# Kernel optimization log

Measured on AMD Instinct MI355X. Metric: run time of the kernel, lower is better.

The kernel has to match this reference:

```python
import jax, jax.numpy as jnp
import numpy as np

B, S, D_MODEL, D_FF = 4, 2048, 1024, 4096


def setup_inputs() -> dict:
    key = jax.random.key(0)
    ks = jax.random.split(key, 8)
    return {
        "x": jax.random.normal(ks[0], (B, S, D_MODEL), dtype=jnp.float32),
        "W1": jax.random.normal(ks[1], (D_MODEL, D_FF), dtype=jnp.float32) * (1.0 / np.sqrt(D_MODEL)),
        "b1": jnp.zeros((D_FF,), dtype=jnp.float32),
        "quantum_phases": jax.random.normal(ks[2], (D_FF,), dtype=jnp.float32) * (2.0 * np.pi),
        "quantum_weights_real": jax.random.normal(ks[3], (D_FF,), dtype=jnp.float32) * 0.1,
        "quantum_weights_imag": jax.random.normal(ks[4], (D_FF,), dtype=jnp.float32) * 0.1,
        "W2": jax.random.normal(ks[5], (D_FF, D_MODEL), dtype=jnp.float32) * (1.0 / np.sqrt(D_FF)),
        "b2": jnp.zeros((D_MODEL,), dtype=jnp.float32),
    }


def _quantum_transform(hidden, theta, w_real, w_imag):
    # hidden: [B,S,d_ff]; theta/w_real/w_imag: [d_ff] broadcast over channels
    imag = w_imag * jnp.sin(theta + hidden * 0.1)
    quantum_phase = jnp.cos(theta) * w_real + jnp.sin(theta) * w_imag  # [d_ff]
    return hidden + quantum_phase * imag * 0.1


def reference(x, W1, b1, quantum_phases, quantum_weights_real, quantum_weights_imag, W2, b2):
    hidden = jnp.einsum("bsd,df->bsf", x, W1) + b1  # [B,S,d_ff]
    q = _quantum_transform(hidden, quantum_phases, quantum_weights_real, quantum_weights_imag)
    act = jax.nn.relu(q)  # dropout is identity in eval mode
    return jnp.einsum("bsf,fd->bsd", act, W2) + b2
```

## Files before the change

kernel.cpp:

```cpp
#include <hip/hip_runtime.h>

typedef __bf16 bf16x8 __attribute__((ext_vector_type(8)));
typedef short  s16x8  __attribute__((ext_vector_type(8)));
typedef float  f32x4  __attribute__((ext_vector_type(4)));

#define DEVINL __device__ __forceinline__

DEVINL unsigned short f2bf(float f) {
  unsigned int u = __builtin_bit_cast(unsigned int, f);
  u += 0x7fffu + ((u >> 16) & 1u);
  return (unsigned short)(u >> 16);
}

DEVINL void async16(const void* g, void* l) {
  __builtin_amdgcn_global_load_lds(
      (const __attribute__((address_space(1))) unsigned int*)g,
      (__attribute__((address_space(3))) unsigned int*)l, 16, 0, 0);
}


__global__ void cvt_f32_bf16(const float* __restrict__ in,
                             unsigned short* __restrict__ out, int n4) {
  int i = blockIdx.x * blockDim.x + threadIdx.x;
  int stride = gridDim.x * blockDim.x;
  for (; i < n4; i += stride) {
    float4 v = ((const float4*)in)[i];
    ushort4 o;
    o.x = f2bf(v.x); o.y = f2bf(v.y); o.z = f2bf(v.z); o.w = f2bf(v.w);
    ((ushort4*)out)[i] = o;
  }
}

__global__ void transpose_cvt(const float* __restrict__ in,
                              unsigned short* __restrict__ out, int R, int C) {
  __shared__ unsigned short tile[32][33];
  int bc = blockIdx.x * 32, br = blockIdx.y * 32;
  int tx = threadIdx.x & 31, ty = threadIdx.x >> 5;
#pragma unroll
  for (int i = 0; i < 32; i += 8)
    tile[ty + i][tx] = f2bf(in[(size_t)(br + ty + i) * C + (bc + tx)]);
  __syncthreads();
#pragma unroll
  for (int i = 0; i < 32; i += 8)
    out[(size_t)(bc + ty + i) * R + (br + tx)] = tile[tx][ty + i];
}

__global__ void qconst(const float* __restrict__ theta,
                       const float* __restrict__ wre,
                       const float* __restrict__ wim,
                       float* __restrict__ c1, int n) {
  int i = blockIdx.x * blockDim.x + threadIdx.x;
  if (i < n) {
    float t = theta[i];
    c1[i] = (cosf(t) * wre[i] + sinf(t) * wim[i]) * wim[i] * 0.1f;
  }
}


template <int BM, int NT, int REPS, bool FUSED>
__global__ __launch_bounds__(512, 2) void gemm8(
    const unsigned short* __restrict__ A,
    const unsigned short* __restrict__ Bt,
    const float* __restrict__ bias,
    const float* __restrict__ theta,
    const float* __restrict__ c1,
    void* __restrict__ Cout,
    int N, int nTilesN) {
  constexpr int K      = NT * 64;
  constexpr int WROWS  = BM / 2;
  constexpr int M_REP  = WROWS / 16;
  constexpr int MH     = M_REP / 2;
  constexpr int ABYTES = BM * 128;
  constexpr int AH     = ABYTES / 2;
  constexpr int AL     = AH / 8192;
  constexpr int BUFSZ  = ABYTES + 32768;
  constexpr int LDSSZ  = 2 * BUFSZ + (FUSED ? 16384 : 0);
  static_assert(AL == 2 || AL == 1, "geometry");

  __shared__ __align__(16) char lds[LDSSZ];

  int nwg = gridDim.x;
  int wg = blockIdx.x;
  int sw = (wg & 7) * (nwg >> 3) + (wg >> 3);
  int rowBase = (sw / nTilesN) * BM;
  int colBase = (sw % nTilesN) * (256 * REPS);

  const int t = threadIdx.x;
  const int lane = t & 63;
  const int wid = t >> 6;
  const int wr = wid >> 2, wc = wid & 3;
  const int lr = lane & 15;
  const int lg = lane >> 4;
  const int r7 = lane & 7;

  const int srow = t >> 3;
  const int scolB = ((t & 7) * 16) ^ ((srow & 7) << 4);
  const unsigned short* aSrcB = A  + (size_t)(rowBase + srow) * K + (scolB >> 1);
  const unsigned short* bSrcB = Bt + (size_t)(colBase + srow) * K + (scolB >> 1);

  const int aRd = (wr * WROWS + lr) * 128 + ((lg ^ r7) << 4);
  const int bRd = ABYTES + (wc * 64 + lr) * 128 + ((lg ^ r7) << 4);

#define STAGE_AU(S, U, P) do {                                              \
    _Pragma("unroll") for (int j = 0; j < AL; ++j)                          \
      async16(aSrcB + ((size_t)((U) * WROWS + j * 64) * K + (size_t)(S) * 64),\
              &lds[(P) * BUFSZ + (U) * AH + j * 8192 + t * 16]);            \
  } while (0)
#define STAGE_BU(SRC, S, U, P) do {                                         \
    _Pragma("unroll") for (int j = 0; j < 2; ++j)                           \
      async16((SRC) + ((size_t)((U) * 128 + j * 64) * K + (size_t)(S) * 64),\
              &lds[(P) * BUFSZ + ABYTES + (U) * 16384 + j * 8192 + t * 16]);\
  } while (0)

#define LOAD_A(MHh, P)                                                      \
  _Pragma("unroll") for (int mi = 0; mi < MH; ++mi)                         \
  _Pragma("unroll") for (int ks = 0; ks < 2; ++ks)                          \
    a[mi][ks] = __builtin_bit_cast(bf16x8, *(const s16x8*)&lds[             \
        (P) * BUFSZ + ((aRd + ((MHh) * MH + mi) * 2048) ^ (ks << 6))])
#define LOAD_B(NHh, P)                                                      \
  _Pragma("unroll") for (int nn = 0; nn < 2; ++nn)                          \
  _Pragma("unroll") for (int ks = 0; ks < 2; ++ks)                          \
    b[(NHh) * 2 + nn][ks] = __builtin_bit_cast(bf16x8, *(const s16x8*)&lds[ \
        (P) * BUFSZ + ((bRd + ((NHh) * 2 + nn) * 2048) ^ (ks << 6))])

#define QUAD(MHh, NHh)                                                      \
  __builtin_amdgcn_s_setprio(1);                                            \
  _Pragma("unroll") for (int mi = 0; mi < MH; ++mi)                         \
  _Pragma("unroll") for (int nn = 0; nn < 2; ++nn)                          \
  _Pragma("unroll") for (int ks = 0; ks < 2; ++ks)                          \
    acc[(MHh) * MH + mi][(NHh) * 2 + nn] =                                  \
        __builtin_amdgcn_mfma_f32_16x16x32_bf16(                            \
            a[mi][ks], b[(NHh) * 2 + nn][ks],                               \
            acc[(MHh) * MH + mi][(NHh) * 2 + nn], 0, 0, 0);                 \
  __builtin_amdgcn_s_setprio(0)

#define BAR() __builtin_amdgcn_s_barrier()
#define LG0() asm volatile("s_waitcnt lgkmcnt(0)" ::: "memory")

#define TILE(T, P) do {                                                     \
    LOAD_A(0, P); LOAD_B(0, P);                                             \
    if ((T) + 1 < NT) STAGE_AU((T) + 1, 0, (P) ^ 1);                        \
    if (MH == 4) asm volatile("s_waitcnt lgkmcnt(8)" ::: "memory");         \
    BAR(); LG0(); QUAD(0, 0); BAR();                                        \
    LOAD_B(1, P);                                                           \
    if ((T) + 1 < NT) STAGE_AU((T) + 1, 1, (P) ^ 1);                        \
    BAR(); LG0(); QUAD(0, 1); BAR();                                        \
    LOAD_A(1, P);                                                           \
    if ((T) + 2 < NT) STAGE_BU(bSrcR, (T) + 2, 0, P);                       \
    BAR(); LG0(); QUAD(1, 1); BAR();                                        \
    if ((T) + 2 < NT) STAGE_BU(bSrcR, (T) + 2, 1, P);                       \
    BAR(); QUAD(1, 0);                                                      \
    if ((T) + 2 < NT) {                                                     \
      asm volatile("s_waitcnt vmcnt(4)" ::: "memory");                      \
    } else if ((T) + 1 < NT) {                                              \
      asm volatile("s_waitcnt vmcnt(0)" ::: "memory");                      \
    }                                                                       \
    BAR();                                                                  \
  } while (0)

  STAGE_AU(0, 0, 0); STAGE_AU(0, 1, 0);
  STAGE_BU(bSrcB, 0, 0, 0); STAGE_BU(bSrcB, 0, 1, 0);
  STAGE_BU(bSrcB, 1, 0, 1); STAGE_BU(bSrcB, 1, 1, 1);
  asm volatile("s_waitcnt vmcnt(4)" ::: "memory");
  BAR();

  for (int rep = 0; rep < REPS; ++rep) {
    const unsigned short* bSrcR = bSrcB + (size_t)rep * 256 * K;
    f32x4 acc[M_REP][4] = {};
    bf16x8 a[MH][2], b[4][2];

    for (int T = 0; T < NT; T += 2) {
      TILE(T, 0);
      TILE(T + 1, 1);
    }

    if (rep + 1 < REPS) {
      const unsigned short* bSrcN = bSrcB + (size_t)(rep + 1) * 256 * K;
      STAGE_AU(0, 0, 0); STAGE_AU(0, 1, 0);
      STAGE_BU(bSrcN, 0, 0, 0); STAGE_BU(bSrcN, 0, 1, 0);
      STAGE_BU(bSrcN, 1, 0, 1); STAGE_BU(bSrcN, 1, 1, 1);
    }

    const int colR = colBase + rep * 256;
    const int ocol0 = colR + wc * 64 + lr;
    if constexpr (FUSED) {
      float bvv[4], thv[4], ccv[4];
#pragma unroll
      for (int ni = 0; ni < 4; ++ni) {
        int n = ocol0 + ni * 16;
        bvv[ni] = bias[n]; thv[ni] = theta[n]; ccv[ni] = c1[n];
      }
      const int SB = 2 * BUFSZ + wid * 2048;
      const int srw = lane >> 2;
      const int sbyte = (lane & 3) * 32;
      const size_t growB = (size_t)(rowBase + wr * WROWS) * N;
      unsigned short* outp = (unsigned short*)Cout;
#pragma unroll
      for (int mi = 0; mi < M_REP; ++mi) {
#pragma unroll
        for (int ni = 0; ni < 4; ++ni) {
#pragma unroll
          for (int r = 0; r < 4; ++r) {
            int row16 = lg * 4 + r;
            float h = acc[mi][ni][r] + bvv[ni];
            float q = h + ccv[ni] * __sinf(thv[ni] + 0.1f * h);
            unsigned short v = f2bf(fmaxf(q, 0.f));
            int ad = SB + row16 * 128 +
                     (((ni * 16 + lr) * 2) ^ ((row16 & 7) << 4));
            *(unsigned short*)&lds[ad] = v;
          }
        }
        s16x8 w0 = *(const s16x8*)&lds[SB + srw * 128 +
                                       ((sbyte) ^ ((srw & 7) << 4))];
        s16x8 w1 = *(const s16x8*)&lds[SB + srw * 128 +
                                       ((sbyte + 16) ^ ((srw & 7) << 4))];
        unsigned short* dst = outp + growB + (size_t)(mi * 16 + srw) * N +
                              colR + wc * 64 + (lane & 3) * 16;
        *(s16x8*)dst = w0;
        *(s16x8*)(dst + 8) = w1;
      }
    } else {
      const int orow0 = rowBase + wr * WROWS + lg * 4;
#pragma unroll
      for (int ni = 0; ni < 4; ++ni) {
        int n = ocol0 + ni * 16;
        float bv = bias[n];
#pragma unroll
        for (int mi = 0; mi < M_REP; ++mi) {
#pragma unroll
          for (int r = 0; r < 4; ++r) {
            size_t m = (size_t)(orow0 + mi * 16 + r);
            ((float*)Cout)[m * N + n] = acc[mi][ni][r] + bv;
          }
        }
      }
    }

    if (rep + 1 < REPS) {
      asm volatile("s_waitcnt vmcnt(0)" ::: "memory");
      BAR();
    }
  }

#undef TILE
#undef QUAD
#undef LOAD_A
#undef LOAD_B
#undef STAGE_AU
#undef STAGE_BU
#undef BAR
#undef LG0
}


extern "C" void kernel_launch(void* const* d_in, const int* in_sizes, int n_in,
                              void* d_out, int out_size, void* d_ws,
                              size_t ws_size, hipStream_t stream) {
  const float* x     = (const float*)d_in[0];
  const float* W1    = (const float*)d_in[1];
  const float* b1    = (const float*)d_in[2];
  const float* theta = (const float*)d_in[3];
  const float* qwr   = (const float*)d_in[4];
  const float* qwi   = (const float*)d_in[5];
  const float* W2    = (const float*)d_in[6];
  const float* b2    = (const float*)d_in[7];
  float* out = (float*)d_out;

  const int M = 4 * 2048;
  const int DM = 1024, DF = 4096;

  size_t need = ((size_t)96 << 20) + DF * sizeof(float);
  if (ws_size < need) return;

  char* ws = (char*)d_ws;
  unsigned short* xb   = (unsigned short*)ws;
  unsigned short* w1t  = (unsigned short*)(ws + ((size_t)16 << 20));
  unsigned short* w2t  = (unsigned short*)(ws + ((size_t)24 << 20));
  unsigned short* actb = (unsigned short*)(ws + ((size_t)32 << 20));
  float* c1 = (float*)(ws + ((size_t)96 << 20));

  cvt_f32_bf16<<<2048, 256, 0, stream>>>(x, xb, M * DM / 4);
  transpose_cvt<<<dim3(DF / 32, DM / 32), 256, 0, stream>>>(W1, w1t, DM, DF);
  transpose_cvt<<<dim3(DM / 32, DF / 32), 256, 0, stream>>>(W2, w2t, DF, DM);
  qconst<<<DF / 256, 256, 0, stream>>>(theta, qwr, qwi, c1, DF);

  gemm8<256, 16, 2, true><<<256, 512, 0, stream>>>(
      xb, w1t, b1, theta, c1, (void*)actb, DF, DF / 512);
  gemm8<128, 64, 1, false><<<256, 512, 0, stream>>>(
      actb, w2t, b2, nullptr, nullptr, (void*)out, DM, DM / 256);
}
```

Before: 168.7 us.

## Fuse prep kernels into one launch and stage GEMM epilogues through LDS

The four preprocessing kernels (x conversion, two weight transposes, phase constants) become one launch with block-range dispatch, which cuts launch overhead. The template GEMM is split into two specialized kernels. The second GEMM's fp32 output now goes through swizzled LDS so it can be written as coalesced 16-byte vector stores, replacing the scattered scalar stores. The first GEMM's epilogue store pattern is also reshaped. The cost is extra LDS and a larger fused prep grid.

```diff
diff --git a/kernel.cpp b/kernel.cpp
--- a/kernel.cpp
+++ b/kernel.cpp
@@ -19,71 +19,74 @@
 }
 
 
-__global__ void cvt_f32_bf16(const float* __restrict__ in,
-                             unsigned short* __restrict__ out, int n4) {
-  int i = blockIdx.x * blockDim.x + threadIdx.x;
-  int stride = gridDim.x * blockDim.x;
-  for (; i < n4; i += stride) {
-    float4 v = ((const float4*)in)[i];
-    ushort4 o;
-    o.x = f2bf(v.x); o.y = f2bf(v.y); o.z = f2bf(v.z); o.w = f2bf(v.w);
-    ((ushort4*)out)[i] = o;
-  }
-}
-
-__global__ void transpose_cvt(const float* __restrict__ in,
-                              unsigned short* __restrict__ out, int R, int C) {
+__global__ __launch_bounds__(256) void prep(
+    const float* __restrict__ x, const float* __restrict__ W1,
+    const float* __restrict__ W2, const float* __restrict__ theta,
+    const float* __restrict__ wre, const float* __restrict__ wim,
+    unsigned short* __restrict__ xb, unsigned short* __restrict__ w1t,
+    unsigned short* __restrict__ w2t, float* __restrict__ c1) {
   __shared__ unsigned short tile[32][33];
-  int bc = blockIdx.x * 32, br = blockIdx.y * 32;
-  int tx = threadIdx.x & 31, ty = threadIdx.x >> 5;
-#pragma unroll
-  for (int i = 0; i < 32; i += 8)
-    tile[ty + i][tx] = f2bf(in[(size_t)(br + ty + i) * C + (bc + tx)]);
-  __syncthreads();
-#pragma unroll
-  for (int i = 0; i < 32; i += 8)
-    out[(size_t)(bc + ty + i) * R + (br + tx)] = tile[tx][ty + i];
-}
-
-__global__ void qconst(const float* __restrict__ theta,
-                       const float* __restrict__ wre,
-                       const float* __restrict__ wim,
-                       float* __restrict__ c1, int n) {
-  int i = blockIdx.x * blockDim.x + threadIdx.x;
-  if (i < n) {
+  const int b = blockIdx.x;
+  const int tid = threadIdx.x;
+  if (b < 1024) {
+    int i = b * 256 + tid;
+#pragma unroll
+    for (int k = 0; k < 8; ++k, i += 262144) {
+      float4 v = ((const float4*)x)[i];
+      ushort4 o;
+      o.x = f2bf(v.x); o.y = f2bf(v.y); o.z = f2bf(v.z); o.w = f2bf(v.w);
+      ((ushort4*)xb)[i] = o;
+    }
+  } else if (b < 5120) {
+    int bb = b - 1024;
+    int bc = (bb & 127) * 32, br = (bb >> 7) * 32;
+    int tx = tid & 31, ty = tid >> 5;
+#pragma unroll
+    for (int i = 0; i < 32; i += 8)
+      tile[ty + i][tx] = f2bf(W1[(size_t)(br + ty + i) * 4096 + (bc + tx)]);
+    __syncthreads();
+#pragma unroll
+    for (int i = 0; i < 32; i += 8)
+      w1t[(size_t)(bc + ty + i) * 1024 + (br + tx)] = tile[tx][ty + i];
+  } else if (b < 9216) {
+    int bb = b - 5120;
+    int bc = (bb & 31) * 32, br = (bb >> 5) * 32;
+    int tx = tid & 31, ty = tid >> 5;
+#pragma unroll
+    for (int i = 0; i < 32; i += 8)
+      tile[ty + i][tx] = f2bf(W2[(size_t)(br + ty + i) * 1024 + (bc + tx)]);
+    __syncthreads();
+#pragma unroll
+    for (int i = 0; i < 32; i += 8)
+      w2t[(size_t)(bc + ty + i) * 4096 + (br + tx)] = tile[tx][ty + i];
+  } else {
+    int i = (b - 9216) * 256 + tid;
     float t = theta[i];
     c1[i] = (cosf(t) * wre[i] + sinf(t) * wim[i]) * wim[i] * 0.1f;
   }
 }
 
 
-template <int BM, int NT, int REPS, bool FUSED>
-__global__ __launch_bounds__(512, 2) void gemm8(
+__global__ __launch_bounds__(512, 2) void gemm1k(
     const unsigned short* __restrict__ A,
     const unsigned short* __restrict__ Bt,
     const float* __restrict__ bias,
     const float* __restrict__ theta,
     const float* __restrict__ c1,
-    void* __restrict__ Cout,
-    int N, int nTilesN) {
-  constexpr int K      = NT * 64;
-  constexpr int WROWS  = BM / 2;
-  constexpr int M_REP  = WROWS / 16;
-  constexpr int MH     = M_REP / 2;
-  constexpr int ABYTES = BM * 128;
-  constexpr int AH     = ABYTES / 2;
-  constexpr int AL     = AH / 8192;
-  constexpr int BUFSZ  = ABYTES + 32768;
-  constexpr int LDSSZ  = 2 * BUFSZ + (FUSED ? 16384 : 0);
-  static_assert(AL == 2 || AL == 1, "geometry");
-
-  __shared__ __align__(16) char lds[LDSSZ];
+    unsigned short* __restrict__ Cout) {
+  constexpr int K = 1024, N = 4096, NT = 16, REPS = 2;
+  constexpr int WROWS = 128, M_REP = 8, MH = 4;
+  constexpr int ABYTES = 32768, AH = 16384, AL = 2;
+  constexpr int BUFSZ = 65536;
+  constexpr int nTilesN = 8;
+
+  __shared__ __align__(16) char lds[2 * BUFSZ + 16384];
 
   int nwg = gridDim.x;
   int wg = blockIdx.x;
   int sw = (wg & 7) * (nwg >> 3) + (wg >> 3);
-  int rowBase = (sw / nTilesN) * BM;
-  int colBase = (sw % nTilesN) * (256 * REPS);
+  int rowBase = (sw / nTilesN) * 256;
+  int colBase = (sw % nTilesN) * 512;
 
   const int t = threadIdx.x;
   const int lane = t & 63;
@@ -111,7 +114,6 @@
       async16((SRC) + ((size_t)((U) * 128 + j * 64) * K + (size_t)(S) * 64),\
               &lds[(P) * BUFSZ + ABYTES + (U) * 16384 + j * 8192 + t * 16]);\
   } while (0)
-
 #define LOAD_A(MHh, P)                                                      \
   _Pragma("unroll") for (int mi = 0; mi < MH; ++mi)                         \
   _Pragma("unroll") for (int ks = 0; ks < 2; ++ks)                          \
@@ -122,7 +124,6 @@
   _Pragma("unroll") for (int ks = 0; ks < 2; ++ks)                          \
     b[(NHh) * 2 + nn][ks] = __builtin_bit_cast(bf16x8, *(const s16x8*)&lds[ \
         (P) * BUFSZ + ((bRd + ((NHh) * 2 + nn) * 2048) ^ (ks << 6))])
-
 #define QUAD(MHh, NHh)                                                      \
   __builtin_amdgcn_s_setprio(1);                                            \
   _Pragma("unroll") for (int mi = 0; mi < MH; ++mi)                         \
@@ -133,14 +134,12 @@
             a[mi][ks], b[(NHh) * 2 + nn][ks],                               \
             acc[(MHh) * MH + mi][(NHh) * 2 + nn], 0, 0, 0);                 \
   __builtin_amdgcn_s_setprio(0)
-
 #define BAR() __builtin_amdgcn_s_barrier()
 #define LG0() asm volatile("s_waitcnt lgkmcnt(0)" ::: "memory")
-
 #define TILE(T, P) do {                                                     \
     LOAD_A(0, P); LOAD_B(0, P);                                             \
     if ((T) + 1 < NT) STAGE_AU((T) + 1, 0, (P) ^ 1);                        \
-    if (MH == 4) asm volatile("s_waitcnt lgkmcnt(8)" ::: "memory");         \
+    asm volatile("s_waitcnt lgkmcnt(8)" ::: "memory");                      \
     BAR(); LG0(); QUAD(0, 0); BAR();                                        \
     LOAD_B(1, P);                                                           \
     if ((T) + 1 < NT) STAGE_AU((T) + 1, 1, (P) ^ 1);                        \
@@ -183,57 +182,38 @@
 
     const int colR = colBase + rep * 256;
     const int ocol0 = colR + wc * 64 + lr;
-    if constexpr (FUSED) {
-      float bvv[4], thv[4], ccv[4];
+    float bvv[4], thv[4], ccv[4];
+#pragma unroll
+    for (int ni = 0; ni < 4; ++ni) {
+      int n = ocol0 + ni * 16;
+      bvv[ni] = bias[n]; thv[ni] = theta[n]; ccv[ni] = c1[n];
+    }
+    const int SB = 2 * BUFSZ + wid * 2048;
+    const size_t growB = (size_t)(rowBase + wr * WROWS) * N;
+    const int rd = lane >> 3;
+    const int bo = (lane & 7) * 16;
+#pragma unroll
+    for (int mi = 0; mi < M_REP; ++mi) {
 #pragma unroll
       for (int ni = 0; ni < 4; ++ni) {
-        int n = ocol0 + ni * 16;
-        bvv[ni] = bias[n]; thv[ni] = theta[n]; ccv[ni] = c1[n];
-      }
-      const int SB = 2 * BUFSZ + wid * 2048;
-      const int srw = lane >> 2;
-      const int sbyte = (lane & 3) * 32;
-      const size_t growB = (size_t)(rowBase + wr * WROWS) * N;
-      unsigned short* outp = (unsigned short*)Cout;
-#pragma unroll
-      for (int mi = 0; mi < M_REP; ++mi) {
-#pragma unroll
-        for (int ni = 0; ni < 4; ++ni) {
-#pragma unroll
-          for (int r = 0; r < 4; ++r) {
-            int row16 = lg * 4 + r;
-            float h = acc[mi][ni][r] + bvv[ni];
-            float q = h + ccv[ni] * __sinf(thv[ni] + 0.1f * h);
-            unsigned short v = f2bf(fmaxf(q, 0.f));
-            int ad = SB + row16 * 128 +
-                     (((ni * 16 + lr) * 2) ^ ((row16 & 7) << 4));
-            *(unsigned short*)&lds[ad] = v;
-          }
-        }
-        s16x8 w0 = *(const s16x8*)&lds[SB + srw * 128 +
-                                       ((sbyte) ^ ((srw & 7) << 4))];
-        s16x8 w1 = *(const s16x8*)&lds[SB + srw * 128 +
-                                       ((sbyte + 16) ^ ((srw & 7) << 4))];
-        unsigned short* dst = outp + growB + (size_t)(mi * 16 + srw) * N +
-                              colR + wc * 64 + (lane & 3) * 16;
-        *(s16x8*)dst = w0;
-        *(s16x8*)(dst + 8) = w1;
-      }
-    } else {
-      const int orow0 = rowBase + wr * WROWS + lg * 4;
-#pragma unroll
-      for (int ni = 0; ni < 4; ++ni) {
-        int n = ocol0 + ni * 16;
-        float bv = bias[n];
-#pragma unroll
-        for (int mi = 0; mi < M_REP; ++mi) {
-#pragma unroll
-          for (int r = 0; r < 4; ++r) {
-            size_t m = (size_t)(orow0 + mi * 16 + r);
-            ((float*)Cout)[m * N + n] = acc[mi][ni][r] + bv;
-          }
+#pragma unroll
+        for (int r = 0; r < 4; ++r) {
+          int row16 = lg * 4 + r;
+          float h = acc[mi][ni][r] + bvv[ni];
+          float q = h + ccv[ni] * __sinf(thv[ni] + 0.1f * h);
+          unsigned short v = f2bf(fmaxf(q, 0.f));
+          int ad = SB + row16 * 128 +
+                   (((ni * 16 + lr) * 2) ^ ((row16 & 7) << 4));
+          *(unsigned short*)&lds[ad] = v;
         }
       }
+      s16x8 w0 = *(const s16x8*)&lds[SB + rd * 128 + (bo ^ ((rd & 7) << 4))];
+      s16x8 w1 = *(const s16x8*)&lds[SB + (rd + 8) * 128 +
+                                     (bo ^ ((rd & 7) << 4))];
+      unsigned short* dst = Cout + growB + (size_t)(mi * 16 + rd) * N +
+                            colR + wc * 64 + (lane & 7) * 8;
+      *(s16x8*)dst = w0;
+      *(s16x8*)(dst + (size_t)8 * N) = w1;
     }
 
     if (rep + 1 < REPS) {
@@ -241,7 +221,6 @@
       BAR();
     }
   }
-
 #undef TILE
 #undef QUAD
 #undef LOAD_A
@@ -250,6 +229,153 @@
 #undef STAGE_BU
 #undef BAR
 #undef LG0
+}
+
+
+__global__ __launch_bounds__(512, 2) void gemm2k(
+    const unsigned short* __restrict__ A,
+    const unsigned short* __restrict__ Bt,
+    const float* __restrict__ bias,
+    float* __restrict__ Cout) {
+  constexpr int K = 4096, N = 1024, NT = 64;
+  constexpr int WROWS = 64, M_REP = 4, MH = 2;
+  constexpr int ABYTES = 16384, AH = 8192, AL = 1;
+  constexpr int BUFSZ = 49152;
+  constexpr int nTilesN = 4;
+
+  __shared__ __align__(16) char lds[2 * BUFSZ + 32768];
+
+  int nwg = gridDim.x;
+  int wg = blockIdx.x;
+  int sw = (wg & 7) * (nwg >> 3) + (wg >> 3);
+  int rowBase = (sw / nTilesN) * 128;
+  int colBase = (sw % nTilesN) * 256;
+
+  const int t = threadIdx.x;
+  const int lane = t & 63;
+  const int wid = t >> 6;
+  const int wr = wid >> 2, wc = wid & 3;
+  const int lr = lane & 15;
+  const int lg = lane >> 4;
+  const int r7 = lane & 7;
+
+  const int srow = t >> 3;
+  const int scolB = ((t & 7) * 16) ^ ((srow & 7) << 4);
+  const unsigned short* aSrcB = A  + (size_t)(rowBase + srow) * K + (scolB >> 1);
+  const unsigned short* bSrcB = Bt + (size_t)(colBase + srow) * K + (scolB >> 1);
+
+  const int aRd = (wr * WROWS + lr) * 128 + ((lg ^ r7) << 4);
+  const int bRd = ABYTES + (wc * 64 + lr) * 128 + ((lg ^ r7) << 4);
+
+  f32x4 acc[M_REP][4] = {};
+  bf16x8 a[MH][2], b[4][2];
+
+#define STAGE_AU(S, U, P) do {                                              \
+    _Pragma("unroll") for (int j = 0; j < AL; ++j)                          \
+      async16(aSrcB + ((size_t)((U) * WROWS + j * 64) * K + (size_t)(S) * 64),\
+              &lds[(P) * BUFSZ + (U) * AH + j * 8192 + t * 16]);            \
+  } while (0)
+#define STAGE_BU(S, U, P) do {                                              \
+    _Pragma("unroll") for (int j = 0; j < 2; ++j)                           \
+      async16(bSrcB + ((size_t)((U) * 128 + j * 64) * K + (size_t)(S) * 64),\
+              &lds[(P) * BUFSZ + ABYTES + (U) * 16384 + j * 8192 + t * 16]);\
+  } while (0)
+#define LOAD_A(MHh, P)                                                      \
+  _Pragma("unroll") for (int mi = 0; mi < MH; ++mi)                         \
+  _Pragma("unroll") for (int ks = 0; ks < 2; ++ks)                          \
+    a[mi][ks] = __builtin_bit_cast(bf16x8, *(const s16x8*)&lds[             \
+        (P) * BUFSZ + ((aRd + ((MHh) * MH + mi) * 2048) ^ (ks << 6))])
+#define LOAD_B(NHh, P)                                                      \
+  _Pragma("unroll") for (int nn = 0; nn < 2; ++nn)                          \
+  _Pragma("unroll") for (int ks = 0; ks < 2; ++ks)                          \
+    b[(NHh) * 2 + nn][ks] = __builtin_bit_cast(bf16x8, *(const s16x8*)&lds[ \
+        (P) * BUFSZ + ((bRd + ((NHh) * 2 + nn) * 2048) ^ (ks << 6))])
+#define QUAD(MHh, NHh)                                                      \
+  __builtin_amdgcn_s_setprio(1);                                            \
+  _Pragma("unroll") for (int mi = 0; mi < MH; ++mi)                         \
+  _Pragma("unroll") for (int nn = 0; nn < 2; ++nn)                          \
+  _Pragma("unroll") for (int ks = 0; ks < 2; ++ks)                          \
+    acc[(MHh) * MH + mi][(NHh) * 2 + nn] =                                  \
+        __builtin_amdgcn_mfma_f32_16x16x32_bf16(                            \
+            a[mi][ks], b[(NHh) * 2 + nn][ks],                               \
+            acc[(MHh) * MH + mi][(NHh) * 2 + nn], 0, 0, 0);                 \
+  __builtin_amdgcn_s_setprio(0)
+#define BAR() __builtin_amdgcn_s_barrier()
+#define LG0() asm volatile("s_waitcnt lgkmcnt(0)" ::: "memory")
+#define TILE(T, P) do {                                                     \
+    LOAD_A(0, P); LOAD_B(0, P);                                             \
+    if ((T) + 1 < NT) STAGE_AU((T) + 1, 0, (P) ^ 1);                        \
+    BAR(); LG0(); QUAD(0, 0); BAR();                                        \
+    LOAD_B(1, P);                                                           \
+    if ((T) + 1 < NT) STAGE_AU((T) + 1, 1, (P) ^ 1);                        \
+    BAR(); LG0(); QUAD(0, 1); BAR();                                        \
+    LOAD_A(1, P);                                                           \
+    if ((T) + 2 < NT) STAGE_BU((T) + 2, 0, P);                              \
+    BAR(); LG0(); QUAD(1, 1); BAR();                                        \
+    if ((T) + 2 < NT) STAGE_BU((T) + 2, 1, P);                              \
+    BAR(); QUAD(1, 0);                                                      \
+    if ((T) + 2 < NT) {                                                     \
+      asm volatile("s_waitcnt vmcnt(4)" ::: "memory");                      \
+    } else if ((T) + 1 < NT) {                                              \
+      asm volatile("s_waitcnt vmcnt(0)" ::: "memory");                      \
+    }                                                                       \
+    BAR();                                                                  \
+  } while (0)
+
+  STAGE_AU(0, 0, 0); STAGE_AU(0, 1, 0);
+  STAGE_BU(0, 0, 0); STAGE_BU(0, 1, 0);
+  STAGE_BU(1, 0, 1); STAGE_BU(1, 1, 1);
+  asm volatile("s_waitcnt vmcnt(4)" ::: "memory");
+  BAR();
+
+  for (int T = 0; T < NT; T += 2) {
+    TILE(T, 0);
+    TILE(T + 1, 1);
+  }
+#undef TILE
+#undef QUAD
+#undef LOAD_A
+#undef LOAD_B
+#undef STAGE_AU
+#undef STAGE_BU
+#undef BAR
+#undef LG0
+
+  const int ocol0 = colBase + wc * 64 + lr;
+  float bvv[4];
+#pragma unroll
+  for (int ni = 0; ni < 4; ++ni) bvv[ni] = bias[ocol0 + ni * 16];
+  const int SB = 2 * BUFSZ + wid * 4096;
+  const int orowB = rowBase + wr * WROWS;
+  const int rd = lane >> 3;
+  const int bo = (lane & 7) * 16;
+#pragma unroll
+  for (int mi = 0; mi < M_REP; ++mi) {
+#pragma unroll
+    for (int ni = 0; ni < 4; ++ni) {
+#pragma unroll
+      for (int r = 0; r < 4; ++r) {
+        int row16 = lg * 4 + r;
+        int ad = SB + row16 * 256 +
+                 (((ni * 16 + lr) * 4) ^ ((row16 & 7) << 4));
+        *(float*)&lds[ad] = acc[mi][ni][r] + bvv[ni];
+      }
+    }
+    f32x4 v00 = *(const f32x4*)&lds[SB + rd * 256 + (bo ^ ((rd & 7) << 4))];
+    f32x4 v01 = *(const f32x4*)&lds[SB + rd * 256 +
+                                    ((bo + 128) ^ ((rd & 7) << 4))];
+    f32x4 v10 = *(const f32x4*)&lds[SB + (rd + 8) * 256 +
+                                    (bo ^ ((rd & 7) << 4))];
+    f32x4 v11 = *(const f32x4*)&lds[SB + (rd + 8) * 256 +
+                                    ((bo + 128) ^ ((rd & 7) << 4))];
+    float* dst0 = Cout + (size_t)(orowB + mi * 16 + rd) * N +
+                  colBase + wc * 64 + (lane & 7) * 4;
+    *(f32x4*)dst0 = v00;
+    *(f32x4*)(dst0 + 32) = v01;
+    float* dst1 = dst0 + (size_t)8 * N;
+    *(f32x4*)dst1 = v10;
+    *(f32x4*)(dst1 + 32) = v11;
+  }
 }
 
 
@@ -266,9 +392,7 @@
   const float* b2    = (const float*)d_in[7];
   float* out = (float*)d_out;
 
-  const int M = 4 * 2048;
-  const int DM = 1024, DF = 4096;
-
+  const int DF = 4096;
   size_t need = ((size_t)96 << 20) + DF * sizeof(float);
   if (ws_size < need) return;
 
@@ -279,13 +403,8 @@
   unsigned short* actb = (unsigned short*)(ws + ((size_t)32 << 20));
   float* c1 = (float*)(ws + ((size_t)96 << 20));
 
-  cvt_f32_bf16<<<2048, 256, 0, stream>>>(x, xb, M * DM / 4);
-  transpose_cvt<<<dim3(DF / 32, DM / 32), 256, 0, stream>>>(W1, w1t, DM, DF);
-  transpose_cvt<<<dim3(DM / 32, DF / 32), 256, 0, stream>>>(W2, w2t, DF, DM);
-  qconst<<<DF / 256, 256, 0, stream>>>(theta, qwr, qwi, c1, DF);
-
-  gemm8<256, 16, 2, true><<<256, 512, 0, stream>>>(
-      xb, w1t, b1, theta, c1, (void*)actb, DF, DF / 512);
-  gemm8<128, 64, 1, false><<<256, 512, 0, stream>>>(
-      actb, w2t, b2, nullptr, nullptr, (void*)out, DM, DM / 256);
-}
+  prep<<<9232, 256, 0, stream>>>(x, W1, W2, theta, qwr, qwi,
+                                 xb, w1t, w2t, c1);
+  gemm1k<<<256, 512, 0, stream>>>(xb, w1t, b1, theta, c1, actb);
+  gemm2k<<<256, 512, 0, stream>>>(actb, w2t, b2, out);
+}
```

After: 154.5 us. -8.4%, faster.
